# Kernel tuning notes

Hardware: AMD Instinct MI355X
Metric: run time of the kernel (lower is better)

## Reference

```python
import jax, jax.numpy as jnp
import numpy as np

N_NODES = 50000
N_EDGES = 600000
N_PAIRS = 200000
F_ATOM = 64
F_PAIR = 32
HID = 128
N_LAYERS = 3
EPS = 1e-5


def setup_inputs() -> dict:
    key = jax.random.key(0)
    ks = jax.random.split(key, 24)
    d = {}
    d["atom_features"] = jax.random.normal(ks[0], (N_NODES, F_ATOM), jnp.float32)
    d["edge_index"] = jax.random.randint(ks[1], (2, N_EDGES), 0, N_NODES)
    d["pair_indices"] = jax.random.randint(ks[2], (N_PAIRS, 2), 0, N_NODES)
    d["pair_features"] = jax.random.normal(ks[3], (N_PAIRS, F_PAIR), jnp.float32)
    # atom embedding linear
    d["embed_W"] = jax.random.normal(ks[4], (F_ATOM, HID), jnp.float32) / np.sqrt(F_ATOM)
    d["embed_b"] = jnp.zeros((HID,), jnp.float32)
    # stacked GCNConv weights [L, HID, HID]
    d["conv_W"] = jax.random.normal(ks[5], (N_LAYERS, HID, HID), jnp.float32) / np.sqrt(HID)
    d["conv_b"] = jnp.zeros((N_LAYERS, HID), jnp.float32)
    # BatchNorm (eval mode: running stats)
    d["bn_gamma"] = jnp.ones((N_LAYERS, HID), jnp.float32)
    d["bn_beta"] = jnp.zeros((N_LAYERS, HID), jnp.float32)
    d["bn_mean"] = jax.random.normal(ks[6], (N_LAYERS, HID), jnp.float32) * 0.1
    d["bn_var"] = jax.random.uniform(ks[7], (N_LAYERS, HID), jnp.float32, 0.5, 1.5)
    # pair MLP: Linear(2H+Fp -> H), Linear(H -> H//2), Linear(H//2 -> 1)
    din1 = 2 * HID + F_PAIR
    d["mlp_W1"] = jax.random.normal(ks[8], (din1, HID), jnp.float32) / np.sqrt(din1)
    d["mlp_b1"] = jnp.zeros((HID,), jnp.float32)
    d["mlp_W2"] = jax.random.normal(ks[9], (HID, HID // 2), jnp.float32) / np.sqrt(HID)
    d["mlp_b2"] = jnp.zeros((HID // 2,), jnp.float32)
    d["mlp_W3"] = jax.random.normal(ks[10], (HID // 2, 1), jnp.float32) / np.sqrt(HID // 2)
    d["mlp_b3"] = jnp.zeros((1,), jnp.float32)
    return d


def _gcn_conv(x, W, b, row, col, deg_inv_sqrt):
    # PyG GCNConv: x' = W x, then symmetric-normalized sum aggregation (self-loops
    # already folded into row/col/deg_inv_sqrt).
    h = x @ W  # [N, H]
    norm = deg_inv_sqrt[row] * deg_inv_sqrt[col]  # [E']
    msg = h[col] * norm[:, None]  # [E', H] gather
    out = jax.ops.segment_sum(msg, row, num_segments=x.shape[0])  # scatter-add
    return out + b


def reference(atom_features, edge_index, pair_indices, pair_features,
              embed_W, embed_b, conv_W, conv_b,
              bn_gamma, bn_beta, bn_mean, bn_var,
              mlp_W1, mlp_b1, mlp_W2, mlp_b2, mlp_W3, mlp_b3):
    n = atom_features.shape[0]
    # add self loops once (same for every layer)
    loop = jnp.arange(n, dtype=edge_index.dtype)
    row = jnp.concatenate([edge_index[0], loop])
    col = jnp.concatenate([edge_index[1], loop])
    deg = jax.ops.segment_sum(jnp.ones_like(row, dtype=jnp.float32), row, num_segments=n)
    deg_inv_sqrt = jnp.where(deg > 0, jax.lax.rsqrt(deg), 0.0)

    x = atom_features @ embed_W + embed_b  # [N, H]
    for i in range(N_LAYERS):
        x = _gcn_conv(x, conv_W[i], conv_b[i], row, col, deg_inv_sqrt)
        # BatchNorm1d, eval mode (running stats)
        x = (x - bn_mean[i]) * jax.lax.rsqrt(bn_var[i] + EPS) * bn_gamma[i] + bn_beta[i]
        x = jax.nn.relu(x)
        # dropout: identity in eval mode

    p0 = x[pair_indices[:, 0]]  # [P, H]
    p1 = x[pair_indices[:, 1]]  # [P, H]
    z = jnp.concatenate([p0, p1, pair_features], axis=1)  # [P, 2H+Fp]
    z = jax.nn.relu(z @ mlp_W1 + mlp_b1)
    z = jax.nn.relu(z @ mlp_W2 + mlp_b2)
    return z @ mlp_W3 + mlp_b3  # [P, 1]
```

## Files before the change

### kernel.cpp

```cpp
#include <hip/hip_runtime.h>
#include <hip/hip_bf16.h>
#include <stdint.h>

#define NN 50000
#define NE 600000
#define NP 200000
#define SCAN_CHUNK 1024
#define NB_SCAN ((NN + SCAN_CHUNK - 1) / SCAN_CHUNK)

#define PB_W    400
#define PB_CNT  ((NE + 255) / 256)
#define PB_PF   ((NP * 32 / 8 + 255) / 256)

#define FB_FILL ((NE + 255) / 256)
#define FB_EMB  ((NN + 127) / 128)

typedef __attribute__((ext_vector_type(8))) short short8;
typedef __attribute__((ext_vector_type(4))) float f32x4;

static __device__ __forceinline__ unsigned short f2bf(float f) {
  union { float f; unsigned u; } a; a.f = f;
  unsigned r = a.u + 0x7fff + ((a.u >> 16) & 1);
  return (unsigned short)(r >> 16);
}
static __device__ __forceinline__ float bf2f(unsigned short h) {
  union { unsigned u; float f; } a; a.u = ((unsigned)h) << 16;
  return a.f;
}
static __device__ __forceinline__ float lo16f(unsigned w) {
  union { unsigned u; float f; } a; a.u = w << 16; return a.f;
}
static __device__ __forceinline__ float hi16f(unsigned w) {
  union { unsigned u; float f; } a; a.u = w & 0xffff0000u; return a.f;
}


__global__ __launch_bounds__(256) void prep_all(
    const float* __restrict__ embW, const float* __restrict__ convW,
    const float* __restrict__ W1, const float* __restrict__ W2,
    const int* __restrict__ erow, const float* __restrict__ pf,
    unsigned short* __restrict__ embT, unsigned short* __restrict__ convT,
    unsigned short* __restrict__ W1T, unsigned short* __restrict__ W2T,
    int* __restrict__ counts, unsigned short* __restrict__ pf_bf) {
  const int b = blockIdx.x, t = threadIdx.x;
  if (b < PB_W) {
    int idx = b * 256 + t;
    if (idx < 8192) {
      int n = idx >> 6, k = idx & 63;
      embT[idx] = f2bf(embW[(size_t)k * 128 + n]);
    } else if (idx < 8192 + 49152) {
      int i2 = idx - 8192;
      int l = i2 >> 14, n = (i2 >> 7) & 127, k = i2 & 127;
      convT[i2] = f2bf(convW[(size_t)l * 16384 + (size_t)k * 128 + n]);
    } else if (idx < 8192 + 49152 + 36864) {
      int i3 = idx - 57344;
      int n = i3 / 288, k = i3 % 288;
      W1T[i3] = f2bf(W1[(size_t)k * 128 + n]);
    } else if (idx < 8192 + 49152 + 36864 + 8192) {
      int i4 = idx - 94208;
      int n = i4 >> 7, k = i4 & 127;
      W2T[i4] = f2bf(W2[(size_t)k * 64 + n]);
    }
  } else if (b < PB_W + PB_CNT) {
    int e = (b - PB_W) * 256 + t;
    if (e < NE) atomicAdd(&counts[erow[e]], 1);
  } else {
    int i = (b - PB_W - PB_CNT) * 256 + t;
    if (i < NP * 32 / 8) {
      const float4* s = (const float4*)(pf + (size_t)i * 8);
      float4 v0 = s[0], v1 = s[1];
      short8 o;
      o[0] = (short)f2bf(v0.x); o[1] = (short)f2bf(v0.y);
      o[2] = (short)f2bf(v0.z); o[3] = (short)f2bf(v0.w);
      o[4] = (short)f2bf(v1.x); o[5] = (short)f2bf(v1.y);
      o[6] = (short)f2bf(v1.z); o[7] = (short)f2bf(v1.w);
      *(short8*)(pf_bf + (size_t)i * 8) = o;
    }
  }
}


__global__ __launch_bounds__(256) void scan_partial_dis(const int* __restrict__ counts,
                                                        int* __restrict__ bsum,
                                                        float* __restrict__ dis) {
  const int b = blockIdx.x, t = threadIdx.x;
  const int base = b * SCAN_CHUNK;
  int s = 0;
  for (int j = t; j < SCAN_CHUNK; j += 256) {
    int i = base + j;
    if (i < NN) {
      int cv = counts[i];
      s += cv;
      dis[i] = rsqrtf((float)cv + 1.0f);
    }
  }
  __shared__ int red[4];
#pragma unroll
  for (int off = 32; off; off >>= 1) s += __shfl_down(s, off);
  if ((t & 63) == 0) red[t >> 6] = s;
  __syncthreads();
  if (t == 0) bsum[b] = red[0] + red[1] + red[2] + red[3];
}

__global__ __launch_bounds__(256) void scan_final(const int* __restrict__ counts,
                                                  const int* __restrict__ bsum,
                                                  int* __restrict__ row_ptr,
                                                  int* __restrict__ cursor) {
  const int b = blockIdx.x, t = threadIdx.x;
  __shared__ int sb[64];
  if (t < 64) {
    int v = (t < NB_SCAN) ? bsum[t] : 0;
    int orig = v;
#pragma unroll
    for (int off = 1; off < 64; off <<= 1) {
      int u = __shfl_up(v, off);
      if (t >= off) v += u;
    }
    sb[t] = v - orig;
  }
  const int i0 = b * SCAN_CHUNK + t * 4;
  int c[4]; int s = 0;
#pragma unroll
  for (int r = 0; r < 4; ++r) { int i = i0 + r; c[r] = (i < NN) ? counts[i] : 0; s += c[r]; }
  __shared__ int sc[256];
  sc[t] = s;
  __syncthreads();
  for (int off = 1; off < 256; off <<= 1) {
    int add = (t >= off) ? sc[t - off] : 0;
    __syncthreads();
    sc[t] += add;
    __syncthreads();
  }
  int run = sb[b] + sc[t] - s;
#pragma unroll
  for (int r = 0; r < 4; ++r) {
    int i = i0 + r;
    if (i < NN) { row_ptr[i] = run; cursor[i] = run; run += c[r]; }
  }
  if (b == 0 && t == 0) row_ptr[NN] = NE;
}


__global__ __launch_bounds__(256) void fill_embed(
    const int* __restrict__ erow, const int* __restrict__ ecol,
    int* __restrict__ cursor, int* __restrict__ csr_col,
    const float* __restrict__ atom, const unsigned short* __restrict__ embT,
    const float* __restrict__ embB, const float* __restrict__ dis,
    unsigned short* __restrict__ outb) {
  const int b = blockIdx.x;
  if (b < FB_FILL) {
    int e = b * 256 + threadIdx.x;
    if (e < NE) {
      int r = erow[e];
      int pos = atomicAdd(&cursor[r], 1);
      csr_col[pos] = ecol[e];
    }
    return;
  }
  const int bid  = b - FB_FILL;
  const int K    = 64;
  const int tid  = threadIdx.x;
  const int lane = tid & 63;
  const int w    = tid >> 6;
  const int l15  = lane & 15;
  const int khi  = (lane >> 4) * 8;
  const int rowb = bid * 128 + w * 32;

  int ar[2];
#pragma unroll
  for (int rt = 0; rt < 2; ++rt) {
    int r = rowb + rt * 16 + l15;
    ar[rt] = (r < NN) ? r : NN - 1;
  }

  f32x4 acc[2][8];
#pragma unroll
  for (int rt = 0; rt < 2; ++rt)
#pragma unroll
    for (int ct = 0; ct < 8; ++ct) acc[rt][ct] = (f32x4){0.f, 0.f, 0.f, 0.f};

#pragma unroll
  for (int kb = 0; kb < K; kb += 32) {
    short8 ahi[2], alo[2];
#pragma unroll
    for (int rt = 0; rt < 2; ++rt) {
      const float* asrc = atom + (size_t)ar[rt] * K + kb + khi;
      float4 va0 = *(const float4*)(asrc);
      float4 va1 = *(const float4*)(asrc + 4);
      float av[8] = {va0.x, va0.y, va0.z, va0.w, va1.x, va1.y, va1.z, va1.w};
#pragma unroll
      for (int j = 0; j < 8; ++j) {
        unsigned short h = f2bf(av[j]);
        ahi[rt][j] = (short)h;
        alo[rt][j] = (short)f2bf(av[j] - bf2f(h));
      }
    }
#pragma unroll
    for (int ct = 0; ct < 8; ++ct) {
      short8 bfrag = *(const short8*)(embT + (size_t)(ct * 16 + l15) * K + kb + khi);
#pragma unroll
      for (int rt = 0; rt < 2; ++rt) {
        acc[rt][ct] = __builtin_amdgcn_mfma_f32_16x16x32_bf16(ahi[rt], bfrag, acc[rt][ct], 0, 0, 0);
        acc[rt][ct] = __builtin_amdgcn_mfma_f32_16x16x32_bf16(alo[rt], bfrag, acc[rt][ct], 0, 0, 0);
      }
    }
  }

#pragma unroll
  for (int rt = 0; rt < 2; ++rt) {
    const int orow0 = rowb + rt * 16 + (lane >> 4) * 4;
    float dv[4];
#pragma unroll
    for (int r = 0; r < 4; ++r) dv[r] = (orow0 + r < NN) ? dis[orow0 + r] : 0.f;
#pragma unroll
    for (int ct = 0; ct < 8; ++ct) {
      int col = ct * 16 + l15;
      float bb = embB[col];
#pragma unroll
      for (int r = 0; r < 4; ++r) {
        int orow = orow0 + r;
        if (orow < NN) {
          float v = (acc[rt][ct][r] + bb) * dv[r];
          outb[(size_t)orow * 128 + col] = f2bf(v);
        }
      }
    }
  }
}


__global__ __launch_bounds__(256) void agg4_kernel(const unsigned short* __restrict__ xsb,
    const int* __restrict__ row_ptr, const int* __restrict__ csr_col,
    const float* __restrict__ dis, unsigned short* __restrict__ y_bf) {
  const int t = threadIdx.x;
  const int n = blockIdx.x * 4 + (t >> 6);
  if (n >= NN) return;
  const int l    = t & 63;
  const int half = l >> 5;
  const int cl   = l & 31;
  const uint2* xs2 = (const uint2*)xsb;

  float a0, a1, a2, a3;
  {
    uint2 v = make_uint2(0u, 0u);
    if (half == 0) v = xs2[(size_t)n * 32 + cl];
    a0 = lo16f(v.x); a1 = hi16f(v.x);
    a2 = lo16f(v.y); a3 = hi16f(v.y);
  }

  const int s = row_ptr[n], e = row_ptr[n + 1];
  for (int j0 = s; j0 < e; j0 += 16) {
    int idx[8];
#pragma unroll
    for (int q = 0; q < 8; ++q) {
      int j = j0 + 2 * q + half;
      idx[q] = (j < e) ? csr_col[j] : -1;
    }
    uint2 ww[8];
#pragma unroll
    for (int q = 0; q < 8; ++q) {
      int r = (idx[q] < 0) ? 0 : idx[q];
      ww[q] = xs2[(size_t)r * 32 + cl];
    }
#pragma unroll
    for (int q = 0; q < 8; ++q) {
      if (idx[q] < 0) { ww[q].x = 0u; ww[q].y = 0u; }
      a0 += lo16f(ww[q].x); a1 += hi16f(ww[q].x);
      a2 += lo16f(ww[q].y); a3 += hi16f(ww[q].y);
    }
  }

  a0 += __shfl_xor(a0, 32);
  a1 += __shfl_xor(a1, 32);
  a2 += __shfl_xor(a2, 32);
  a3 += __shfl_xor(a3, 32);

  if (half == 0) {
    float dv = dis[n];
    uint2 o;
    o.x = (unsigned)f2bf(dv * a0) | ((unsigned)f2bf(dv * a1) << 16);
    o.y = (unsigned)f2bf(dv * a2) | ((unsigned)f2bf(dv * a3) << 16);
    ((uint2*)y_bf)[(size_t)n * 32 + cl] = o;
  }
}


template<int MODE>
__global__ __launch_bounds__(256) void conv_gemm(
    const unsigned short* __restrict__ Ab,
    const unsigned short* __restrict__ BT,
    const float* __restrict__ bias, const float* __restrict__ dis,
    const float* __restrict__ g, const float* __restrict__ be,
    const float* __restrict__ mn, const float* __restrict__ vr,
    unsigned short* __restrict__ outb) {
  const int K    = 128;
  const int tid  = threadIdx.x;
  const int lane = tid & 63;
  const int w    = tid >> 6;
  const int l15  = lane & 15;
  const int khi  = (lane >> 4) * 8;
  const int rowb = blockIdx.x * 128 + w * 32;

  int ar[2];
#pragma unroll
  for (int rt = 0; rt < 2; ++rt) {
    int r = rowb + rt * 16 + l15;
    ar[rt] = (r < NN) ? r : NN - 1;
  }

  f32x4 acc[2][8];
#pragma unroll
  for (int rt = 0; rt < 2; ++rt)
#pragma unroll
    for (int ct = 0; ct < 8; ++ct) acc[rt][ct] = (f32x4){0.f, 0.f, 0.f, 0.f};

#pragma unroll
  for (int kb = 0; kb < K; kb += 32) {
    short8 afr[2];
#pragma unroll
    for (int rt = 0; rt < 2; ++rt)
      afr[rt] = *(const short8*)(Ab + (size_t)ar[rt] * K + kb + khi);
#pragma unroll
    for (int ct = 0; ct < 8; ++ct) {
      short8 bfrag = *(const short8*)(BT + (size_t)(ct * 16 + l15) * K + kb + khi);
#pragma unroll
      for (int rt = 0; rt < 2; ++rt)
        acc[rt][ct] = __builtin_amdgcn_mfma_f32_16x16x32_bf16(afr[rt], bfrag, acc[rt][ct], 0, 0, 0);
    }
  }

#pragma unroll
  for (int rt = 0; rt < 2; ++rt) {
    const int orow0 = rowb + rt * 16 + (lane >> 4) * 4;
    float dv[4];
    if constexpr (MODE == 1) {
#pragma unroll
      for (int r = 0; r < 4; ++r) dv[r] = (orow0 + r < NN) ? dis[orow0 + r] : 0.f;
    }
#pragma unroll
    for (int ct = 0; ct < 8; ++ct) {
      int col = ct * 16 + l15;
      float bb = bias[col];
      float inv = rsqrtf(vr[col] + 1e-5f);
      float scale = g[col] * inv;
      float shift = be[col] - mn[col] * scale;
#pragma unroll
      for (int r = 0; r < 4; ++r) {
        int orow = orow0 + r;
        if (orow < NN) {
          float v = fmaxf((acc[rt][ct][r] + bb) * scale + shift, 0.f);
          if constexpr (MODE == 1) v *= dv[r];
          outb[(size_t)orow * 128 + col] = f2bf(v);
        }
      }
    }
  }
}


__global__ __launch_bounds__(256, 3) void mlp2_kernel(
    const unsigned short* __restrict__ xb, const int* __restrict__ pairs,
    const unsigned short* __restrict__ pfb,
    const unsigned short* __restrict__ W1T, const float* __restrict__ b1,
    const unsigned short* __restrict__ W2T, const float* __restrict__ b2,
    const float* __restrict__ W3, const float* __restrict__ b3,
    float* __restrict__ out) {
  __shared__ unsigned short H1[128 * 136];

  const int tid  = threadIdx.x;
  const int lane = tid & 63;
  const int w    = tid >> 6;
  const int pb   = blockIdx.x * 128;
  const int rowbase = w * 32;
  const int l15  = lane & 15;
  const int khi  = (lane >> 4) * 8;
  const int rq   = (lane >> 4) * 4;

  int gp0 = pb + rowbase + l15;       if (gp0 >= NP) gp0 = NP - 1;
  int gp1 = pb + rowbase + 16 + l15;  if (gp1 >= NP) gp1 = NP - 1;
  const int2 pr0 = ((const int2*)pairs)[gp0];
  const int2 pr1 = ((const int2*)pairs)[gp1];

  short8 af[18];
#pragma unroll
  for (int kb = 0; kb < 4; ++kb) {
    af[kb]     = *(const short8*)(xb + (size_t)pr0.x * 128 + kb * 32 + khi);
    af[4 + kb] = *(const short8*)(xb + (size_t)pr0.y * 128 + kb * 32 + khi);
    af[9 + kb]     = *(const short8*)(xb + (size_t)pr1.x * 128 + kb * 32 + khi);
    af[9 + 4 + kb] = *(const short8*)(xb + (size_t)pr1.y * 128 + kb * 32 + khi);
  }
  af[8]  = *(const short8*)(pfb + (size_t)gp0 * 32 + khi);
  af[17] = *(const short8*)(pfb + (size_t)gp1 * 32 + khi);

  f32x4 acc[2][8];
#pragma unroll
  for (int p = 0; p < 2; ++p)
#pragma unroll
    for (int c = 0; c < 8; ++c) acc[p][c] = (f32x4){0.f, 0.f, 0.f, 0.f};

#pragma unroll
  for (int kb = 0; kb < 9; ++kb) {
    const unsigned short* wrow = W1T + (size_t)kb * 32 + khi;
#pragma unroll
    for (int ct = 0; ct < 8; ++ct) {
      short8 bfrag = *(const short8*)(wrow + (size_t)(ct * 16 + l15) * 288);
      acc[0][ct] = __builtin_amdgcn_mfma_f32_16x16x32_bf16(af[kb], bfrag, acc[0][ct], 0, 0, 0);
      acc[1][ct] = __builtin_amdgcn_mfma_f32_16x16x32_bf16(af[9 + kb], bfrag, acc[1][ct], 0, 0, 0);
    }
  }

#pragma unroll
  for (int ct = 0; ct < 8; ++ct) {
    float bv = b1[ct * 16 + l15];
    int col = ct * 16 + l15;
#pragma unroll
    for (int p = 0; p < 2; ++p) {
#pragma unroll
      for (int r = 0; r < 4; ++r) {
        int row = rowbase + p * 16 + rq + r;
        float v = fmaxf(acc[p][ct][r] + bv, 0.f);
        H1[row * 136 + col] = f2bf(v);
      }
    }
  }
  __syncthreads();

  f32x4 acc2[2][4];
#pragma unroll
  for (int p = 0; p < 2; ++p)
#pragma unroll
    for (int c = 0; c < 4; ++c) acc2[p][c] = (f32x4){0.f, 0.f, 0.f, 0.f};

#pragma unroll
  for (int kb = 0; kb < 4; ++kb) {
    int ko = kb * 32 + khi;
    short8 a0 = *(const short8*)&H1[(rowbase + l15) * 136 + ko];
    short8 a1 = *(const short8*)&H1[(rowbase + 16 + l15) * 136 + ko];
    const unsigned short* wrow = W2T + (size_t)ko;
#pragma unroll
    for (int ct = 0; ct < 4; ++ct) {
      short8 bfrag = *(const short8*)(wrow + (size_t)(ct * 16 + l15) * 128);
      acc2[0][ct] = __builtin_amdgcn_mfma_f32_16x16x32_bf16(a0, bfrag, acc2[0][ct], 0, 0, 0);
      acc2[1][ct] = __builtin_amdgcn_mfma_f32_16x16x32_bf16(a1, bfrag, acc2[1][ct], 0, 0, 0);
    }
  }

  float w3v[4], b2v[4];
#pragma unroll
  for (int ct = 0; ct < 4; ++ct) {
    w3v[ct] = W3[ct * 16 + l15];
    b2v[ct] = b2[ct * 16 + l15];
  }
  float b3v = b3[0];
#pragma unroll
  for (int p = 0; p < 2; ++p) {
#pragma unroll
    for (int r = 0; r < 4; ++r) {
      float s = 0.f;
#pragma unroll
      for (int ct = 0; ct < 4; ++ct) {
        float h2 = fmaxf(acc2[p][ct][r] + b2v[ct], 0.f);
        s += h2 * w3v[ct];
      }
      s += __shfl_xor(s, 1);
      s += __shfl_xor(s, 2);
      s += __shfl_xor(s, 4);
      s += __shfl_xor(s, 8);
      int row = pb + rowbase + p * 16 + rq + r;
      if (l15 == 0 && row < NP) out[row] = s + b3v;
    }
  }
}


extern "C" void kernel_launch(void* const* d_in, const int* in_sizes, int n_in,
                              void* d_out, int out_size, void* d_ws, size_t ws_size,
                              hipStream_t stream) {
  (void)in_sizes; (void)n_in; (void)out_size; (void)ws_size;
  const float* atom  = (const float*)d_in[0];
  const int*   eidx  = (const int*)d_in[1];
  const int*   pairs = (const int*)d_in[2];
  const float* pfeat = (const float*)d_in[3];
  const float* embW  = (const float*)d_in[4];
  const float* embB  = (const float*)d_in[5];
  const float* convW = (const float*)d_in[6];
  const float* convB = (const float*)d_in[7];
  const float* bng   = (const float*)d_in[8];
  const float* bnb   = (const float*)d_in[9];
  const float* bnm   = (const float*)d_in[10];
  const float* bnv   = (const float*)d_in[11];
  const float* W1    = (const float*)d_in[12];
  const float* b1    = (const float*)d_in[13];
  const float* W2    = (const float*)d_in[14];
  const float* b2    = (const float*)d_in[15];
  const float* W3    = (const float*)d_in[16];
  const float* b3    = (const float*)d_in[17];
  float* out = (float*)d_out;

  uintptr_t base = (uintptr_t)d_ws;
  auto alloc = [&](size_t bytes) -> uintptr_t {
    uintptr_t p = base;
    base += (bytes + 255) & ~(size_t)255;
    return p;
  };
  int*   counts  = (int*)alloc((size_t)NN * 4);
  int*   row_ptr = (int*)alloc((size_t)(NN + 1) * 4);
  int*   cursor  = (int*)alloc((size_t)NN * 4);
  int*   csr_col = (int*)alloc((size_t)NE * 4);
  float* dis     = (float*)alloc((size_t)NN * 4);
  int*   bsum    = (int*)alloc(64 * 4);
  unsigned short* xs_bf = (unsigned short*)alloc((size_t)NN * 128 * 2);
  unsigned short* y_bf  = (unsigned short*)alloc((size_t)NN * 128 * 2);
  unsigned short* pf_bf = (unsigned short*)alloc((size_t)NP * 32 * 2);
  unsigned short* embT  = (unsigned short*)alloc(8192 * 2);
  unsigned short* convT = (unsigned short*)alloc(49152 * 2);
  unsigned short* W1T   = (unsigned short*)alloc(36864 * 2);
  unsigned short* W2T   = (unsigned short*)alloc(8192 * 2);

  const int* erow = eidx;
  const int* ecol = eidx + NE;

  hipMemsetAsync(counts, 0, (size_t)NN * 4, stream);
  prep_all<<<PB_W + PB_CNT + PB_PF, 256, 0, stream>>>(
      embW, convW, W1, W2, erow, pfeat,
      embT, convT, W1T, W2T, counts, pf_bf);
  scan_partial_dis<<<NB_SCAN, 256, 0, stream>>>(counts, bsum, dis);
  scan_final<<<NB_SCAN, 256, 0, stream>>>(counts, bsum, row_ptr, cursor);

  fill_embed<<<FB_FILL + FB_EMB, 256, 0, stream>>>(
      erow, ecol, cursor, csr_col, atom, embT, embB, dis, xs_bf);

  for (int l = 0; l < 3; ++l) {
    agg4_kernel<<<(NN + 3) / 4, 256, 0, stream>>>(xs_bf, row_ptr, csr_col, dis, y_bf);
    if (l < 2) {
      conv_gemm<1><<<(NN + 127) / 128, 256, 0, stream>>>(
          y_bf, convT + (size_t)l * 16384, convB + (size_t)l * 128, dis,
          bng + (size_t)l * 128, bnb + (size_t)l * 128,
          bnm + (size_t)l * 128, bnv + (size_t)l * 128, xs_bf);
    } else {
      conv_gemm<2><<<(NN + 127) / 128, 256, 0, stream>>>(
          y_bf, convT + (size_t)l * 16384, convB + (size_t)l * 128, nullptr,
          bng + (size_t)l * 128, bnb + (size_t)l * 128,
          bnm + (size_t)l * 128, bnv + (size_t)l * 128, xs_bf);
    }
  }

  mlp2_kernel<<<(NP + 127) / 128, 256, 0, stream>>>(xs_bf, pairs, pf_bf,
                                                    W1T, b1, W2T, b2, W3, b3, out);
}
```

Measured before the change: 323.3 us.

## Build CSR via row-bucketed staging and per-bucket LDS scatter

Instead of one global atomic per edge on a per-row cursor followed by a scattered write of csr_col, edges are first binned by row>>10 into 49 staging buckets, using LDS histograms and one global atomic per bucket per block. Each bucket is then placed into CSR order inside shared memory with LDS atomics and written out coalesced. This aims to cut global-atomic contention and random global writes when building the CSR. It adds an extra pass over the edges and a staging buffer. It also assumes each bucket holds at most 16384 edges and that column indices fit in 16 bits, which holds only for roughly uniform edge distributions.

```diff
diff --git a/kernel.cpp b/kernel.cpp
--- a/kernel.cpp
+++ b/kernel.cpp
@@ -8,12 +8,17 @@
 #define SCAN_CHUNK 1024
 #define NB_SCAN ((NN + SCAN_CHUNK - 1) / SCAN_CHUNK)
 
+#define NBUK 49
+#define BCAP 16384
+#define EPB  2048
+#define PB_BKT ((NE + EPB - 1) / EPB)
+
 #define PB_W    400
 #define PB_CNT  ((NE + 255) / 256)
 #define PB_PF   ((NP * 32 / 8 + 255) / 256)
 
-#define FB_FILL ((NE + 255) / 256)
-#define FB_EMB  ((NN + 127) / 128)
+#define CB_CSR NBUK
+#define CB_EMB ((NN + 127) / 128)
 
 typedef __attribute__((ext_vector_type(8))) short short8;
 typedef __attribute__((ext_vector_type(4))) float f32x4;
@@ -38,10 +43,12 @@
 __global__ __launch_bounds__(256) void prep_all(
     const float* __restrict__ embW, const float* __restrict__ convW,
     const float* __restrict__ W1, const float* __restrict__ W2,
-    const int* __restrict__ erow, const float* __restrict__ pf,
+    const int* __restrict__ erow, const int* __restrict__ ecol,
+    const float* __restrict__ pf,
     unsigned short* __restrict__ embT, unsigned short* __restrict__ convT,
     unsigned short* __restrict__ W1T, unsigned short* __restrict__ W2T,
-    int* __restrict__ counts, unsigned short* __restrict__ pf_bf) {
+    int* __restrict__ counts, unsigned short* __restrict__ pf_bf,
+    int* __restrict__ bcur, unsigned* __restrict__ staging) {
   const int b = blockIdx.x, t = threadIdx.x;
   if (b < PB_W) {
     int idx = b * 256 + t;
@@ -64,7 +71,7 @@
   } else if (b < PB_W + PB_CNT) {
     int e = (b - PB_W) * 256 + t;
     if (e < NE) atomicAdd(&counts[erow[e]], 1);
-  } else {
+  } else if (b < PB_W + PB_CNT + PB_PF) {
     int i = (b - PB_W - PB_CNT) * 256 + t;
     if (i < NP * 32 / 8) {
       const float4* s = (const float4*)(pf + (size_t)i * 8);
@@ -75,6 +82,35 @@
       o[4] = (short)f2bf(v1.x); o[5] = (short)f2bf(v1.y);
       o[6] = (short)f2bf(v1.z); o[7] = (short)f2bf(v1.w);
       *(short8*)(pf_bf + (size_t)i * 8) = o;
+    }
+  } else {
+    __shared__ int hist[NBUK];
+    __shared__ int base[NBUK];
+    const int bb = b - (PB_W + PB_CNT + PB_PF);
+    const int e0 = bb * EPB;
+    for (int i = t; i < NBUK; i += 256) hist[i] = 0;
+    __syncthreads();
+    int rr[8], cc8[8], off8[8];
+#pragma unroll
+    for (int q = 0; q < 8; ++q) {
+      int e = e0 + q * 256 + t;
+      rr[q] = -1;
+      if (e < NE) {
+        rr[q] = erow[e];
+        cc8[q] = ecol[e];
+        off8[q] = atomicAdd(&hist[rr[q] >> 10], 1);
+      }
+    }
+    __syncthreads();
+    for (int i = t; i < NBUK; i += 256) base[i] = atomicAdd(&bcur[i], hist[i]);
+    __syncthreads();
+#pragma unroll
+    for (int q = 0; q < 8; ++q) {
+      if (rr[q] >= 0) {
+        int bk = rr[q] >> 10;
+        staging[(size_t)bk * BCAP + base[bk] + off8[q]] =
+            ((unsigned)rr[q] << 16) | (unsigned)cc8[q];
+      }
     }
   }
 }
@@ -104,8 +140,7 @@
 
 __global__ __launch_bounds__(256) void scan_final(const int* __restrict__ counts,
                                                   const int* __restrict__ bsum,
-                                                  int* __restrict__ row_ptr,
-                                                  int* __restrict__ cursor) {
+                                                  int* __restrict__ row_ptr) {
   const int b = blockIdx.x, t = threadIdx.x;
   __shared__ int sb[64];
   if (t < 64) {
@@ -135,29 +170,41 @@
 #pragma unroll
   for (int r = 0; r < 4; ++r) {
     int i = i0 + r;
-    if (i < NN) { row_ptr[i] = run; cursor[i] = run; run += c[r]; }
+    if (i < NN) { row_ptr[i] = run; run += c[r]; }
   }
   if (b == 0 && t == 0) row_ptr[NN] = NE;
 }
 
 
-__global__ __launch_bounds__(256) void fill_embed(
-    const int* __restrict__ erow, const int* __restrict__ ecol,
-    int* __restrict__ cursor, int* __restrict__ csr_col,
+__global__ __launch_bounds__(256) void csr_embed(
+    const int* __restrict__ bcur, const unsigned* __restrict__ staging,
+    const int* __restrict__ row_ptr, int* __restrict__ csr_col,
     const float* __restrict__ atom, const unsigned short* __restrict__ embT,
     const float* __restrict__ embB, const float* __restrict__ dis,
     unsigned short* __restrict__ outb) {
-  const int b = blockIdx.x;
-  if (b < FB_FILL) {
-    int e = b * 256 + threadIdx.x;
-    if (e < NE) {
-      int r = erow[e];
-      int pos = atomicAdd(&cursor[r], 1);
-      csr_col[pos] = ecol[e];
-    }
+  if (blockIdx.x < CB_CSR) {
+    __shared__ unsigned short lcsr[BCAP];
+    __shared__ int lcur[1024];
+    const int bk = blockIdx.x, t = threadIdx.x;
+    const int lo = bk << 10;
+    const int hi = (lo + 1024 < NN) ? lo + 1024 : NN;
+    const int segbase = row_ptr[lo];
+    for (int n = lo + t; n < hi; n += 256) lcur[n - lo] = row_ptr[n] - segbase;
+    __syncthreads();
+    const int cnt = bcur[bk];
+    const unsigned* st = staging + (size_t)bk * BCAP;
+    for (int j = t; j < cnt; j += 256) {
+      unsigned rc = st[j];
+      int pos = atomicAdd(&lcur[(rc >> 16) - lo], 1);
+      lcsr[pos] = (unsigned short)(rc & 0xFFFFu);
+    }
+    __syncthreads();
+    const int seglen = row_ptr[hi] - segbase;
+    for (int j = t; j < seglen; j += 256)
+      csr_col[segbase + j] = (int)lcsr[j];
     return;
   }
-  const int bid  = b - FB_FILL;
+  const int bid  = blockIdx.x - CB_CSR;
   const int K    = 64;
   const int tid  = threadIdx.x;
   const int lane = tid & 63;
@@ -503,12 +550,13 @@
     base += (bytes + 255) & ~(size_t)255;
     return p;
   };
-  int*   counts  = (int*)alloc((size_t)NN * 4);
-  int*   row_ptr = (int*)alloc((size_t)(NN + 1) * 4);
-  int*   cursor  = (int*)alloc((size_t)NN * 4);
-  int*   csr_col = (int*)alloc((size_t)NE * 4);
-  float* dis     = (float*)alloc((size_t)NN * 4);
-  int*   bsum    = (int*)alloc(64 * 4);
+  int*      counts  = (int*)alloc((size_t)NN * 4);
+  int*      row_ptr = (int*)alloc((size_t)(NN + 1) * 4);
+  int*      csr_col = (int*)alloc((size_t)NE * 4);
+  float*    dis     = (float*)alloc((size_t)NN * 4);
+  int*      bsum    = (int*)alloc(64 * 4);
+  int*      bcur    = (int*)alloc(64 * 4);
+  unsigned* staging = (unsigned*)alloc((size_t)NBUK * BCAP * 4);
   unsigned short* xs_bf = (unsigned short*)alloc((size_t)NN * 128 * 2);
   unsigned short* y_bf  = (unsigned short*)alloc((size_t)NN * 128 * 2);
   unsigned short* pf_bf = (unsigned short*)alloc((size_t)NP * 32 * 2);
@@ -521,14 +569,15 @@
   const int* ecol = eidx + NE;
 
   hipMemsetAsync(counts, 0, (size_t)NN * 4, stream);
-  prep_all<<<PB_W + PB_CNT + PB_PF, 256, 0, stream>>>(
-      embW, convW, W1, W2, erow, pfeat,
-      embT, convT, W1T, W2T, counts, pf_bf);
+  hipMemsetAsync(bcur, 0, 64 * 4, stream);
+  prep_all<<<PB_W + PB_CNT + PB_PF + PB_BKT, 256, 0, stream>>>(
+      embW, convW, W1, W2, erow, ecol, pfeat,
+      embT, convT, W1T, W2T, counts, pf_bf, bcur, staging);
   scan_partial_dis<<<NB_SCAN, 256, 0, stream>>>(counts, bsum, dis);
-  scan_final<<<NB_SCAN, 256, 0, stream>>>(counts, bsum, row_ptr, cursor);
-
-  fill_embed<<<FB_FILL + FB_EMB, 256, 0, stream>>>(
-      erow, ecol, cursor, csr_col, atom, embT, embB, dis, xs_bf);
+  scan_final<<<NB_SCAN, 256, 0, stream>>>(counts, bsum, row_ptr);
+
+  csr_embed<<<CB_CSR + CB_EMB, 256, 0, stream>>>(
+      bcur, staging, row_ptr, csr_col, atom, embT, embB, dis, xs_bf);
 
   for (int l = 0; l < 3; ++l) {
     agg4_kernel<<<(NN + 3) / 4, 256, 0, stream>>>(xs_bf, row_ptr, csr_col, dis, y_bf);
```

Result: faster. 290.0 us (-10.3%).
